# Kernel optimization log

Measured on AMD Instinct MI355X. Metric: run time of the kernel, lower is better.

## Reference

```python
import jax, jax.numpy as jnp
import numpy as np

NUM_TYPES = 100
D_MODEL = 256
EPS = 1e-5


def setup_inputs() -> dict:
    key = jax.random.key(0)
    ks = jax.random.split(key, 8)
    N = 524288
    z = jax.random.randint(ks[0], (N,), 0, NUM_TYPES)
    x = jax.random.normal(ks[1], (N, 3), dtype=jnp.float32)
    emb = jax.random.normal(ks[2], (NUM_TYPES, D_MODEL), dtype=jnp.float32)
    w1 = jax.random.normal(ks[3], (3, D_MODEL), dtype=jnp.float32) * (1.0 / np.sqrt(3.0))
    b1 = jnp.zeros((D_MODEL,), dtype=jnp.float32)
    w2 = jax.random.normal(ks[4], (D_MODEL, D_MODEL), dtype=jnp.float32) * (1.0 / np.sqrt(D_MODEL))
    b2 = jnp.zeros((D_MODEL,), dtype=jnp.float32)
    gamma = jnp.ones((D_MODEL,), dtype=jnp.float32)
    beta = jnp.zeros((D_MODEL,), dtype=jnp.float32)
    return {"z": z, "x": x, "emb": emb, "w1": w1, "b1": b1,
            "w2": w2, "b2": b2, "gamma": gamma, "beta": beta}


def reference(z, x, emb, w1, b1, w2, b2, gamma, beta):
    # Embedding gather: [N, d]
    h = emb[z]
    # pos MLP: Linear(3,d) -> SiLU -> Linear(d,d)
    p = jnp.dot(x, w1) + b1
    p = jax.nn.silu(p)
    p = jnp.dot(p, w2) + b2
    h = h + p
    # LayerNorm over last dim
    mu = jnp.mean(h, axis=-1, keepdims=True)
    var = jnp.mean(jnp.square(h - mu), axis=-1, keepdims=True)
    h = (h - mu) * jax.lax.rsqrt(var + EPS) * gamma + beta
    return h
```

## Files before the change

kernel.cpp:

```cpp
#include <hip/hip_runtime.h>

#define EPS 1e-5f
#define WAVES 4

typedef __attribute__((ext_vector_type(8)))  short short8;
typedef __attribute__((ext_vector_type(4)))  short short4_t;
typedef __attribute__((ext_vector_type(16))) float f32x16;
typedef __attribute__((ext_vector_type(4)))  float f32x4;

__device__ inline unsigned f2bf(float f) {
    unsigned u = __builtin_bit_cast(unsigned, f);
    return (u + 0x7fffu + ((u >> 16) & 1u)) >> 16;
}

__global__ void prep_w2(const float* __restrict__ w2, unsigned short* __restrict__ w2f) {
    int idx  = blockIdx.x * 256 + threadIdx.x;
    int e    = idx & 7;
    int lane = (idx >> 3) & 63;
    int ks   = (idx >> 9) & 15;
    int nf   = idx >> 13;
    int k    = ks * 16 + (lane >> 5) * 8 + e;
    int n    = nf * 32 + (lane & 31);
    w2f[idx] = (unsigned short)f2bf(w2[k * 256 + n]);
}

__global__ __launch_bounds__(256, 2) void fused_kernel(
    const int* __restrict__ z, const float* __restrict__ x,
    const float* __restrict__ emb, const float* __restrict__ w1,
    const float* __restrict__ b1, const unsigned short* __restrict__ w2f,
    const float* __restrict__ b2, const float* __restrict__ gamma,
    const float* __restrict__ beta, float* __restrict__ out, int N)
{
    __shared__ char  p_lds[WAVES * 16384];
    __shared__ float x_lds[WAVES][32][4];
    __shared__ int   z_lds[WAVES][32];

    const int tid  = threadIdx.x;
    const int wave = tid >> 6;
    const int lane = tid & 63;
    const int l31  = lane & 31;
    const int h    = lane >> 5;
    char* pbuf = p_lds + wave * 16384;

    const int tiles = N >> 5;
    const int t = blockIdx.x * WAVES + wave;
    if (t >= tiles) return;
    const int R = t << 5;

    if (lane < 32) {
        int r = R + lane;
        x_lds[wave][lane][0] = x[r * 3 + 0];
        x_lds[wave][lane][1] = x[r * 3 + 1];
        x_lds[wave][lane][2] = x[r * 3 + 2];
        z_lds[wave][lane]    = z[r];
    }

    f32x16 acc[8];
#pragma unroll
    for (int j = 0; j < 16; ++j) {
        const int rl = (j & 3) + ((j >> 2) << 3) + (h << 2);
        const float* er = emb + (size_t)z_lds[wave][rl] * 256 + l31;
#pragma unroll
        for (int nf = 0; nf < 8; ++nf)
            acc[nf][j] = er[nf * 32];
    }

    const int  c0  = lane * 4;
    const f32x4 w1a = *(const f32x4*)(w1 + c0);
    const f32x4 w1b = *(const f32x4*)(w1 + 256 + c0);
    const f32x4 w1c = *(const f32x4*)(w1 + 512 + c0);
    const f32x4 b1v = *(const f32x4*)(b1 + c0);
    float b2v[8], gv[8], bv[8];
#pragma unroll
    for (int nf = 0; nf < 8; ++nf) {
        int c = nf * 32 + l31;
        b2v[nf] = b2[c]; gv[nf] = gamma[c]; bv[nf] = beta[c];
    }

#pragma unroll
    for (int r = 0; r < 32; ++r) {
        float x0 = x_lds[wave][r][0];
        float x1 = x_lds[wave][r][1];
        float x2 = x_lds[wave][r][2];
        short4_t pv;
#pragma unroll
        for (int j = 0; j < 4; ++j) {
            float tv = x0 * w1a[j] + x1 * w1b[j] + x2 * w1c[j] + b1v[j];
            float s  = tv * __builtin_amdgcn_rcpf(1.f + __expf(-tv));
            pv[j] = (short)f2bf(s);
        }
        int off = (r * 512 + lane * 8) ^ ((r & 7) << 4);
        *(short4_t*)(pbuf + off) = pv;
    }

#pragma unroll
    for (int ks = 0; ks < 16; ++ks) {
        int aoff = (l31 * 512 + ks * 32 + h * 16) ^ ((l31 & 7) << 4);
        short8 a = *(const short8*)(pbuf + aoff);
        const unsigned short* bp = w2f + ks * 512 + lane * 8;
#pragma unroll
        for (int nf = 0; nf < 8; ++nf) {
            short8 b = *(const short8*)(bp + nf * 8192);
            acc[nf] = __builtin_amdgcn_mfma_f32_32x32x16_bf16(a, b, acc[nf], 0, 0, 0);
        }
    }

#pragma unroll
    for (int j = 0; j < 16; ++j) {
        const int rl = (j & 3) + ((j >> 2) << 3) + (h << 2);
        float hv[8];
        float hsum = 0.f, hsq = 0.f;
#pragma unroll
        for (int nf = 0; nf < 8; ++nf) {
            float v = acc[nf][j] + b2v[nf];
            hv[nf] = v; hsum += v; hsq += v * v;
        }
#pragma unroll
        for (int d = 1; d < 32; d <<= 1) {
            hsum += __shfl_xor(hsum, d, 64);
            hsq  += __shfl_xor(hsq,  d, 64);
        }
        float mu  = hsum * (1.f / 256.f);
        float var = hsq * (1.f / 256.f) - mu * mu;
        float rs  = rsqrtf(var + EPS);
        float* orow = out + (size_t)(R + rl) * 256 + l31;
#pragma unroll
        for (int nf = 0; nf < 8; ++nf)
            __builtin_nontemporal_store((hv[nf] - mu) * rs * gv[nf] + bv[nf],
                                        orow + nf * 32);
    }
}

extern "C" void kernel_launch(void* const* d_in, const int* in_sizes, int n_in,
                              void* d_out, int out_size, void* d_ws, size_t ws_size,
                              hipStream_t stream) {
    const int*   z     = (const int*)d_in[0];
    const float* x     = (const float*)d_in[1];
    const float* emb   = (const float*)d_in[2];
    const float* w1    = (const float*)d_in[3];
    const float* b1    = (const float*)d_in[4];
    const float* w2    = (const float*)d_in[5];
    const float* b2    = (const float*)d_in[6];
    const float* gamma = (const float*)d_in[7];
    const float* beta  = (const float*)d_in[8];
    float* out = (float*)d_out;
    const int N = in_sizes[0];

    unsigned short* w2f = (unsigned short*)d_ws;

    prep_w2<<<256, 256, 0, stream>>>(w2, w2f);

    int tiles  = N >> 5;
    int blocks = (tiles + WAVES - 1) / WAVES;
    fused_kernel<<<blocks, 256, 0, stream>>>(z, x, emb, w1, b1, w2f, b2, gamma, beta, out, N);
}
```

Measured before the change: 189.8 us.

## Use persistent grid-stride waves with prefetched inputs and b2 folded into embedding

```diff
diff --git a/kernel.cpp b/kernel.cpp
--- a/kernel.cpp
+++ b/kernel.cpp
@@ -13,23 +13,30 @@
     return (u + 0x7fffu + ((u >> 16) & 1u)) >> 16;
 }
 
-__global__ void prep_w2(const float* __restrict__ w2, unsigned short* __restrict__ w2f) {
-    int idx  = blockIdx.x * 256 + threadIdx.x;
-    int e    = idx & 7;
-    int lane = (idx >> 3) & 63;
-    int ks   = (idx >> 9) & 15;
-    int nf   = idx >> 13;
-    int k    = ks * 16 + (lane >> 5) * 8 + e;
-    int n    = nf * 32 + (lane & 31);
-    w2f[idx] = (unsigned short)f2bf(w2[k * 256 + n]);
+__global__ void prep(const float* __restrict__ w2, const float* __restrict__ emb,
+                     const float* __restrict__ b2,
+                     unsigned short* __restrict__ w2f, float* __restrict__ emb2) {
+    int idx = blockIdx.x * 256 + threadIdx.x;
+    if (idx < 65536) {
+        int e    = idx & 7;
+        int lane = (idx >> 3) & 63;
+        int ks   = (idx >> 9) & 15;
+        int nf   = idx >> 13;
+        int k    = ks * 16 + ((lane >> 5) << 3) + e;
+        int n    = nf * 32 + (lane & 31);
+        w2f[idx] = (unsigned short)f2bf(w2[k * 256 + n]);
+    } else if (idx < 65536 + 25600) {
+        int i = idx - 65536;
+        emb2[i] = emb[i] + b2[i & 255];
+    }
 }
 
 __global__ __launch_bounds__(256, 2) void fused_kernel(
     const int* __restrict__ z, const float* __restrict__ x,
-    const float* __restrict__ emb, const float* __restrict__ w1,
-    const float* __restrict__ b1, const unsigned short* __restrict__ w2f,
-    const float* __restrict__ b2, const float* __restrict__ gamma,
-    const float* __restrict__ beta, float* __restrict__ out, int N)
+    const float* __restrict__ w1, const float* __restrict__ b1,
+    const unsigned short* __restrict__ w2f, const float* __restrict__ emb2,
+    const float* __restrict__ gamma, const float* __restrict__ beta,
+    float* __restrict__ out, int N)
 {
     __shared__ char  p_lds[WAVES * 16384];
     __shared__ float x_lds[WAVES][32][4];
@@ -42,92 +49,111 @@
     const int h    = lane >> 5;
     char* pbuf = p_lds + wave * 16384;
 
-    const int tiles = N >> 5;
-    const int t = blockIdx.x * WAVES + wave;
-    if (t >= tiles) return;
-    const int R = t << 5;
-
-    if (lane < 32) {
-        int r = R + lane;
-        x_lds[wave][lane][0] = x[r * 3 + 0];
-        x_lds[wave][lane][1] = x[r * 3 + 1];
-        x_lds[wave][lane][2] = x[r * 3 + 2];
-        z_lds[wave][lane]    = z[r];
-    }
-
-    f32x16 acc[8];
-#pragma unroll
-    for (int j = 0; j < 16; ++j) {
-        const int rl = (j & 3) + ((j >> 2) << 3) + (h << 2);
-        const float* er = emb + (size_t)z_lds[wave][rl] * 256 + l31;
-#pragma unroll
-        for (int nf = 0; nf < 8; ++nf)
-            acc[nf][j] = er[nf * 32];
-    }
-
     const int  c0  = lane * 4;
     const f32x4 w1a = *(const f32x4*)(w1 + c0);
     const f32x4 w1b = *(const f32x4*)(w1 + 256 + c0);
     const f32x4 w1c = *(const f32x4*)(w1 + 512 + c0);
     const f32x4 b1v = *(const f32x4*)(b1 + c0);
-    float b2v[8], gv[8], bv[8];
+    float gv[8], bv[8];
 #pragma unroll
     for (int nf = 0; nf < 8; ++nf) {
         int c = nf * 32 + l31;
-        b2v[nf] = b2[c]; gv[nf] = gamma[c]; bv[nf] = beta[c];
+        gv[nf] = gamma[c]; bv[nf] = beta[c];
     }
 
-#pragma unroll
-    for (int r = 0; r < 32; ++r) {
-        float x0 = x_lds[wave][r][0];
-        float x1 = x_lds[wave][r][1];
-        float x2 = x_lds[wave][r][2];
-        short4_t pv;
-#pragma unroll
-        for (int j = 0; j < 4; ++j) {
-            float tv = x0 * w1a[j] + x1 * w1b[j] + x2 * w1c[j] + b1v[j];
-            float s  = tv * __builtin_amdgcn_rcpf(1.f + __expf(-tv));
-            pv[j] = (short)f2bf(s);
-        }
-        int off = (r * 512 + lane * 8) ^ ((r & 7) << 4);
-        *(short4_t*)(pbuf + off) = pv;
+    const int tiles  = N >> 5;
+    const int stride = gridDim.x * WAVES;
+    int t = blockIdx.x * WAVES + wave;
+    if (t >= tiles) return;
+
+    float px0 = 0.f, px1 = 0.f, px2 = 0.f; int pz = 0;
+    if (lane < 32) {
+        int r = (t << 5) + lane;
+        px0 = x[r * 3 + 0]; px1 = x[r * 3 + 1]; px2 = x[r * 3 + 2];
+        pz  = z[r];
     }
 
+    for (; t < tiles; t += stride) {
+        const int R = t << 5;
+
+        if (lane < 32) {
+            x_lds[wave][lane][0] = px0;
+            x_lds[wave][lane][1] = px1;
+            x_lds[wave][lane][2] = px2;
+            z_lds[wave][lane]    = pz;
+        }
+
+        f32x16 acc[8];
 #pragma unroll
-    for (int ks = 0; ks < 16; ++ks) {
-        int aoff = (l31 * 512 + ks * 32 + h * 16) ^ ((l31 & 7) << 4);
-        short8 a = *(const short8*)(pbuf + aoff);
-        const unsigned short* bp = w2f + ks * 512 + lane * 8;
+        for (int j = 0; j < 16; ++j) {
+            const int rl = (j & 3) + ((j >> 2) << 3) + (h << 2);
+            const float* er = emb2 + (size_t)z_lds[wave][rl] * 256 + l31;
 #pragma unroll
-        for (int nf = 0; nf < 8; ++nf) {
-            short8 b = *(const short8*)(bp + nf * 8192);
-            acc[nf] = __builtin_amdgcn_mfma_f32_32x32x16_bf16(a, b, acc[nf], 0, 0, 0);
+            for (int nf = 0; nf < 8; ++nf)
+                acc[nf][j] = er[nf * 32];
         }
-    }
 
 #pragma unroll
-    for (int j = 0; j < 16; ++j) {
-        const int rl = (j & 3) + ((j >> 2) << 3) + (h << 2);
-        float hv[8];
-        float hsum = 0.f, hsq = 0.f;
+        for (int r = 0; r < 32; ++r) {
+            float x0 = x_lds[wave][r][0];
+            float x1 = x_lds[wave][r][1];
+            float x2 = x_lds[wave][r][2];
+            short4_t pv;
 #pragma unroll
-        for (int nf = 0; nf < 8; ++nf) {
-            float v = acc[nf][j] + b2v[nf];
-            hv[nf] = v; hsum += v; hsq += v * v;
+            for (int j = 0; j < 4; ++j) {
+                float tv = x0 * w1a[j] + x1 * w1b[j] + x2 * w1c[j] + b1v[j];
+                float s  = tv * __builtin_amdgcn_rcpf(1.f + __expf(-tv));
+                pv[j] = (short)f2bf(s);
+            }
+            int off = (r * 512 + lane * 8) ^ ((r & 7) << 4);
+            *(short4_t*)(pbuf + off) = pv;
         }
+
 #pragma unroll
-        for (int d = 1; d < 32; d <<= 1) {
-            hsum += __shfl_xor(hsum, d, 64);
-            hsq  += __shfl_xor(hsq,  d, 64);
+        for (int ks = 0; ks < 16; ++ks) {
+            int aoff = (l31 * 512 + ks * 32 + h * 16) ^ ((l31 & 7) << 4);
+            short8 a = *(const short8*)(pbuf + aoff);
+            const unsigned short* bp = w2f + ks * 512 + lane * 8;
+#pragma unroll
+            for (int nf = 0; nf < 8; ++nf) {
+                short8 b = *(const short8*)(bp + nf * 8192);
+                acc[nf] = __builtin_amdgcn_mfma_f32_32x32x16_bf16(a, b, acc[nf], 0, 0, 0);
+            }
         }
-        float mu  = hsum * (1.f / 256.f);
-        float var = hsq * (1.f / 256.f) - mu * mu;
-        float rs  = rsqrtf(var + EPS);
-        float* orow = out + (size_t)(R + rl) * 256 + l31;
+
+        {
+            int tn = t + stride;
+            if (tn < tiles && lane < 32) {
+                int r = (tn << 5) + lane;
+                px0 = x[r * 3 + 0]; px1 = x[r * 3 + 1]; px2 = x[r * 3 + 2];
+                pz  = z[r];
+            }
+        }
+
 #pragma unroll
-        for (int nf = 0; nf < 8; ++nf)
-            __builtin_nontemporal_store((hv[nf] - mu) * rs * gv[nf] + bv[nf],
-                                        orow + nf * 32);
+        for (int j = 0; j < 16; ++j) {
+            const int rl = (j & 3) + ((j >> 2) << 3) + (h << 2);
+            float hv[8];
+            float hsum = 0.f, hsq = 0.f;
+#pragma unroll
+            for (int nf = 0; nf < 8; ++nf) {
+                float v = acc[nf][j];
+                hv[nf] = v; hsum += v; hsq += v * v;
+            }
+#pragma unroll
+            for (int d = 1; d < 32; d <<= 1) {
+                hsum += __shfl_xor(hsum, d, 64);
+                hsq  += __shfl_xor(hsq,  d, 64);
+            }
+            float mu  = hsum * (1.f / 256.f);
+            float var = hsq * (1.f / 256.f) - mu * mu;
+            float rs  = rsqrtf(var + EPS);
+            float* orow = out + (size_t)(R + rl) * 256 + l31;
+#pragma unroll
+            for (int nf = 0; nf < 8; ++nf)
+                __builtin_nontemporal_store((hv[nf] - mu) * rs * gv[nf] + bv[nf],
+                                            orow + nf * 32);
+        }
     }
 }
 
@@ -146,11 +172,15 @@
     float* out = (float*)d_out;
     const int N = in_sizes[0];
 
-    unsigned short* w2f = (unsigned short*)d_ws;
+    unsigned short* w2f  = (unsigned short*)d_ws;
+    float*          emb2 = (float*)((char*)d_ws + 131072);
 
-    prep_w2<<<256, 256, 0, stream>>>(w2, w2f);
+    prep<<<(65536 + 25600 + 255) / 256, 256, 0, stream>>>(w2, emb, b2, w2f, emb2);
 
     int tiles  = N >> 5;
-    int blocks = (tiles + WAVES - 1) / WAVES;
-    fused_kernel<<<blocks, 256, 0, stream>>>(z, x, emb, w1, b1, w2f, b2, gamma, beta, out, N);
+    int blocks = 512;
+    int maxb   = (tiles + WAVES - 1) / WAVES;
+    if (blocks > maxb) blocks = maxb;
+    fused_kernel<<<blocks, 256, 0, stream>>>(z, x, w1, b1, w2f, emb2,
+                                             gamma, beta, out, N);
 }
```

Result: slower. 730.5 us (+284.9%).
